# Kernel tuning notes

Hardware: AMD Instinct MI355X
Metric: run time of the kernel (lower is better)

## Reference

```python
import jax, jax.numpy as jnp
from jax import lax
import numpy as np

B, D, T, H = 256, 128, 1024, 64


def setup_inputs() -> dict:
    key = jax.random.key(0)
    ks = jax.random.split(key, 8)
    s = 1.0 / np.sqrt(H)
    latent_chunk = jax.random.normal(ks[0], (B, D, T), dtype=jnp.float32)
    hidden = jnp.zeros((1, B, H), dtype=jnp.float32)
    # PyTorch nn.GRU params: weight_ih [3H, D], weight_hh [3H, H], biases [3H]
    W_ih = jax.random.uniform(ks[1], (3 * H, D), minval=-s, maxval=s, dtype=jnp.float32)
    W_hh = jax.random.uniform(ks[2], (3 * H, H), minval=-s, maxval=s, dtype=jnp.float32)
    b_ih = jax.random.uniform(ks[3], (3 * H,), minval=-s, maxval=s, dtype=jnp.float32)
    b_hh = jax.random.uniform(ks[4], (3 * H,), minval=-s, maxval=s, dtype=jnp.float32)
    head_w = jax.random.uniform(ks[5], (1, H), minval=-s, maxval=s, dtype=jnp.float32)
    head_b = jax.random.uniform(ks[6], (1,), minval=-s, maxval=s, dtype=jnp.float32)
    return {"latent_chunk": latent_chunk, "hidden": hidden, "W_ih": W_ih,
            "W_hh": W_hh, "b_ih": b_ih, "b_hh": b_hh,
            "head_w": head_w, "head_b": head_b}


def _gru_forward(latent_chunk, hidden, W_ih, W_hh, b_ih, b_hh, head_w, head_b):
    # [B, D, T] -> [B, T, D]
    x = jnp.transpose(latent_chunk, (0, 2, 1))
    # Precompute input-gate projections once as a big GEMM: [B, T, 3H]
    xg = jnp.einsum('btd,gd->btg', x, W_ih) + b_ih
    xg_t = jnp.transpose(xg, (1, 0, 2))  # [T, B, 3H] for scan
    h0 = hidden[0]  # single layer: [B, H]

    def step(h, xg_step):
        hg = h @ W_hh.T + b_hh  # [B, 3H]
        xr, xz, xn = jnp.split(xg_step, 3, axis=-1)
        hr, hz, hn = jnp.split(hg, 3, axis=-1)
        r = jax.nn.sigmoid(xr + hr)
        z = jax.nn.sigmoid(xz + hz)
        n = jnp.tanh(xn + r * hn)
        h_new = (1.0 - z) * n + z * h
        return h_new, None

    hT, _ = lax.scan(step, h0, xg_t)
    # last output of single-layer GRU == final hidden state
    log_scale = hT @ head_w.T + head_b  # [B, 1]
    return log_scale, hT[None]  # hidden: [1, B, H]


def reference(latent_chunk, hidden, W_ih, W_hh, b_ih, b_hh, head_w, head_b):
    return _gru_forward(latent_chunk, hidden, W_ih, W_hh, b_ih, b_hh, head_w, head_b)
```

## Files before the change

kernel.cpp:

```cpp
#include <hip/hip_runtime.h>

#define B_ 256
#define D_ 128
#define T_ 1024
#define H_ 64
#define G_ 192
#define TILE_T 64
#define NTILES (T_ / TILE_T)
#define XGS 65
#define KC 32
#define WS 194

typedef float f32x4 __attribute__((ext_vector_type(4)));
typedef unsigned long long u64;

__global__ __launch_bounds__(448, 2) void gru_fused(
    const float* __restrict__ lat, const float* __restrict__ hidden_init,
    const float* __restrict__ W_ih, const float* __restrict__ W_hh,
    const float* __restrict__ b_ih, const float* __restrict__ b_hh,
    const float* __restrict__ head_w, const float* __restrict__ head_b,
    float* __restrict__ out)
{
    __shared__ float xg_s[2][G_ * XGS];
    __shared__ float lat_s[D_ * TILE_T];
    __shared__ float w_s[KC * WS];
    __shared__ float h_priv[3][H_];
    __shared__ u64  slot[3][2][H_];
    __shared__ unsigned prod_done[2], cons_done[2], pbar;

    const int b    = blockIdx.x;
    const int tid  = threadIdx.x;
    const int lane = tid & 63;
    const int wid  = tid >> 6;

    if (tid < 2) { prod_done[tid] = 0u; cons_done[tid] = 0u; }
    if (tid == 2) pbar = 0u;
    if (tid < 192) { slot[tid >> 6][0][tid & 63] = 0ull;
                     slot[tid >> 6][1][tid & 63] = 0ull; }
    __syncthreads();

    if (wid < 3) {
        __builtin_amdgcn_s_setprio(1);
        const int j   = lane;
        const int row = wid * H_ + j;
        f32x4 w4[16];
        {
            const f32x4* W = (const f32x4*)(W_hh + (size_t)row * H_);
#pragma unroll
            for (int q = 0; q < 16; ++q) w4[q] = W[q];
        }
        asm volatile("" : "+v"(w4[0]), "+v"(w4[1]), "+v"(w4[2]), "+v"(w4[3]),
                          "+v"(w4[4]), "+v"(w4[5]), "+v"(w4[6]), "+v"(w4[7]),
                          "+v"(w4[8]), "+v"(w4[9]), "+v"(w4[10]), "+v"(w4[11]),
                          "+v"(w4[12]), "+v"(w4[13]), "+v"(w4[14]), "+v"(w4[15]));
        const float bias = b_hh[row];
        const float hw   = (wid == 0) ? head_w[j] : 0.f;
        const int o1 = (wid == 0) ? 1 : 0;
        const int o2 = (wid == 2) ? 1 : 2;
        float h = hidden_init[b * H_ + j];
        unsigned sg = 0;

        for (int k = 0; k < NTILES; ++k) {
            const int s = k & 1;
            const unsigned tgt = 4u * (unsigned)((k >> 1) + 1);
            while (__hip_atomic_load(&prod_done[s], __ATOMIC_ACQUIRE,
                                     __HIP_MEMORY_SCOPE_WORKGROUP) < tgt)
                __builtin_amdgcn_s_sleep(1);
            const float* xr_p = &xg_s[s][(size_t)j * XGS];
            const float* xz_p = &xg_s[s][(size_t)(H_ + j) * XGS];
            const float* xn_p = &xg_s[s][(size_t)(2 * H_ + j) * XGS];

#pragma unroll 2
            for (int t = 0; t < TILE_T; ++t, ++sg) {
                const int par = (int)(sg & 1u);
                h_priv[wid][j] = h;
                float xr = xr_p[t], xz = xz_p[t], xn = xn_p[t];
                const f32x4* h4 = (const f32x4*)h_priv[wid];
                float a0 = 0.f, a1 = 0.f, a2 = 0.f, a3 = 0.f;
#pragma unroll
                for (int q = 0; q < 16; ++q) {
                    f32x4 hv = h4[q];
                    a0 = fmaf(w4[q].x, hv.x, a0); a1 = fmaf(w4[q].y, hv.y, a1);
                    a2 = fmaf(w4[q].z, hv.z, a2); a3 = fmaf(w4[q].w, hv.w, a3);
                }
                float a = ((a0 + a1) + (a2 + a3)) + bias;
                const unsigned want = sg + 1;

                u64 pk = ((u64)want << 32) | (u64)__builtin_bit_cast(unsigned, a);
                __hip_atomic_store(&slot[wid][par][j], pk, __ATOMIC_RELAXED,
                                   __HIP_MEMORY_SCOPE_WORKGROUP);
                u64 v1, v2;
                do {
                    v1 = __hip_atomic_load(&slot[o1][par][j], __ATOMIC_RELAXED,
                                           __HIP_MEMORY_SCOPE_WORKGROUP);
                    v2 = __hip_atomic_load(&slot[o2][par][j], __ATOMIC_RELAXED,
                                           __HIP_MEMORY_SCOPE_WORKGROUP);
                } while ((unsigned)(v1 >> 32) != want || (unsigned)(v2 >> 32) != want);
                float b1 = __builtin_bit_cast(float, (unsigned)v1);
                float b2 = __builtin_bit_cast(float, (unsigned)v2);

                float ar, az, an;
                if (wid == 0)      { ar = a;  az = b1; an = b2; }
                else if (wid == 1) { ar = b1; az = a;  an = b2; }
                else               { ar = b1; az = b2; an = a;  }

                float r   = __builtin_amdgcn_rcpf(1.f + __expf(-(xr + ar)));
                float z   = __builtin_amdgcn_rcpf(1.f + __expf(-(xz + az)));
                float pre = xn + r * an;
                float n   = fmaf(-2.f, __builtin_amdgcn_rcpf(__expf(2.f * pre) + 1.f), 1.f);
                h = fmaf(z, h - n, n);
            }
            if (lane == 0)
                __hip_atomic_fetch_add(&cons_done[s], 1u, __ATOMIC_RELEASE,
                                       __HIP_MEMORY_SCOPE_WORKGROUP);
        }

        if (wid == 0) {
            out[B_ + b * H_ + j] = h;
            float v = h * hw;
#pragma unroll
            for (int off = 32; off > 0; off >>= 1) v += __shfl_down(v, off);
            if (lane == 0) out[b] = v + head_b[0];
        }
    } else {
        const int p  = tid - 192;
        const int tx = p & 7;
        const int gy = p >> 3;
        const float* latb = lat + (size_t)b * (D_ * T_);
        unsigned phase = 0;

        auto psync = [&]() {
            if ((p & 63) == 0)
                __hip_atomic_fetch_add(&pbar, 1u, __ATOMIC_RELEASE,
                                       __HIP_MEMORY_SCOPE_WORKGROUP);
            ++phase;
            while (__hip_atomic_load(&pbar, __ATOMIC_ACQUIRE,
                                     __HIP_MEMORY_SCOPE_WORKGROUP) < 4u * phase) {}
        };

        float bias[6];
#pragma unroll
        for (int i = 0; i < 6; ++i) bias[i] = b_ih[gy * 6 + i];

        for (int k = 0; k < NTILES; ++k) {
            const int s = k & 1, m = k >> 1;
            if (m >= 1) {
                while (__hip_atomic_load(&cons_done[s], __ATOMIC_ACQUIRE,
                                         __HIP_MEMORY_SCOPE_WORKGROUP) < 3u * (unsigned)m)
                    __builtin_amdgcn_s_sleep(1);
            }
            psync();

#pragma unroll
            for (int i = 0; i < 32; ++i) {
                int f = p + 256 * i;
                int d = f >> 6, t = f & 63;
                lat_s[f] = latb[(size_t)d * T_ + k * TILE_T + t];
            }

            float acc[8][6];
#pragma unroll
            for (int jj = 0; jj < 8; ++jj)
#pragma unroll
                for (int i = 0; i < 6; ++i) acc[jj][i] = 0.f;

            for (int kc = 0; kc < D_; kc += KC) {
                psync();
#pragma unroll
                for (int i = 0; i < (G_ * KC) / 256; ++i) {
                    int f = p + 256 * i;
                    int g = f >> 5, kk = f & 31;
                    w_s[kk * WS + g] = W_ih[(size_t)g * D_ + kc + kk];
                }
                psync();
#pragma unroll 4
                for (int kk = 0; kk < KC; ++kk) {
                    f32x4 l0 = *(const f32x4*)&lat_s[(kc + kk) * 64 + tx * 8];
                    f32x4 l1 = *(const f32x4*)&lat_s[(kc + kk) * 64 + tx * 8 + 4];
                    float2 w0 = *(const float2*)&w_s[kk * WS + gy * 6];
                    float2 w1 = *(const float2*)&w_s[kk * WS + gy * 6 + 2];
                    float2 w2 = *(const float2*)&w_s[kk * WS + gy * 6 + 4];
                    float lv[8] = {l0.x, l0.y, l0.z, l0.w, l1.x, l1.y, l1.z, l1.w};
                    float wv[6] = {w0.x, w0.y, w1.x, w1.y, w2.x, w2.y};
#pragma unroll
                    for (int jj = 0; jj < 8; ++jj)
#pragma unroll
                        for (int i = 0; i < 6; ++i)
                            acc[jj][i] = fmaf(lv[jj], wv[i], acc[jj][i]);
                }
            }

            float* xs = xg_s[s];
#pragma unroll
            for (int i = 0; i < 6; ++i)
#pragma unroll
                for (int jj = 0; jj < 8; ++jj)
                    xs[(size_t)(gy * 6 + i) * XGS + tx * 8 + jj] = acc[jj][i] + bias[i];

            if ((p & 63) == 0)
                __hip_atomic_fetch_add(&prod_done[s], 1u, __ATOMIC_RELEASE,
                                       __HIP_MEMORY_SCOPE_WORKGROUP);
        }
    }
}

extern "C" void kernel_launch(void* const* d_in, const int* in_sizes, int n_in,
                              void* d_out, int out_size, void* d_ws, size_t ws_size,
                              hipStream_t stream)
{
    const float* lat   = (const float*)d_in[0];
    const float* hid0  = (const float*)d_in[1];
    const float* W_ih  = (const float*)d_in[2];
    const float* W_hh  = (const float*)d_in[3];
    const float* b_ih  = (const float*)d_in[4];
    const float* b_hh  = (const float*)d_in[5];
    const float* headw = (const float*)d_in[6];
    const float* headb = (const float*)d_in[7];
    float* out = (float*)d_out;

    gru_fused<<<dim3(B_), dim3(448), 0, stream>>>(
        lat, hid0, W_ih, W_hh, b_ih, b_hh, headw, headb, out);
}
```

Before: 454.3 us.

## Push gate partials into per-consumer slots and vectorize FMAs with packed f32x2

The recurrent warps now write their gate partial sums directly into each peer's paired slot, so every consumer reads both values from adjacent locations in its own slot pair. The old scheme had each warp store to its own slot and poll two separate peers. The producer GEMM switches to f32x2 accumulators so the compiler can emit packed FMA, and it halves the W_ih k-chunk size. Recurrent priority rises to 2 and the matvec uses vector f32x4 accumulation. Together these aim to shorten the serial per-step handshake and speed the input projection. The risks are more frequent producer syncs from the smaller chunk, and relying on volatile accesses instead of atomics for ordering.

```diff
diff --git a/kernel.cpp b/kernel.cpp
--- a/kernel.cpp
+++ b/kernel.cpp
@@ -8,10 +8,11 @@
 #define TILE_T 64
 #define NTILES (T_ / TILE_T)
 #define XGS 65
-#define KC 32
+#define KC 16
 #define WS 194
 
 typedef float f32x4 __attribute__((ext_vector_type(4)));
+typedef float f32x2 __attribute__((ext_vector_type(2)));
 typedef unsigned long long u64;
 
 __global__ __launch_bounds__(448, 2) void gru_fused(
@@ -25,7 +26,7 @@
     __shared__ float lat_s[D_ * TILE_T];
     __shared__ float w_s[KC * WS];
     __shared__ float h_priv[3][H_];
-    __shared__ u64  slot[3][2][H_];
+    __shared__ u64  pairs[3][2][H_][2];
     __shared__ unsigned prod_done[2], cons_done[2], pbar;
 
     const int b    = blockIdx.x;
@@ -35,12 +36,11 @@
 
     if (tid < 2) { prod_done[tid] = 0u; cons_done[tid] = 0u; }
     if (tid == 2) pbar = 0u;
-    if (tid < 192) { slot[tid >> 6][0][tid & 63] = 0ull;
-                     slot[tid >> 6][1][tid & 63] = 0ull; }
+    for (int i = tid; i < 3 * 2 * H_ * 2; i += 448) ((u64*)pairs)[i] = 0ull;
     __syncthreads();
 
     if (wid < 3) {
-        __builtin_amdgcn_s_setprio(1);
+        __builtin_amdgcn_s_setprio(2);
         const int j   = lane;
         const int row = wid * H_ + j;
         f32x4 w4[16];
@@ -57,6 +57,12 @@
         const float hw   = (wid == 0) ? head_w[j] : 0.f;
         const int o1 = (wid == 0) ? 1 : 0;
         const int o2 = (wid == 2) ? 1 : 2;
+        const int i1 = (wid < 3 - o1 - wid) ? 0 : 1;
+        const int i2 = (wid < 3 - o2 - wid) ? 0 : 1;
+        volatile u64* wr1 = &pairs[o1][0][j][i1];
+        volatile u64* wr2 = &pairs[o2][0][j][i2];
+        volatile u64* rd  = &pairs[wid][0][j][0];
+        const int pstride = 2 * H_;
         float h = hidden_init[b * H_ + j];
         unsigned sg = 0;
 
@@ -76,25 +82,20 @@
                 h_priv[wid][j] = h;
                 float xr = xr_p[t], xz = xz_p[t], xn = xn_p[t];
                 const f32x4* h4 = (const f32x4*)h_priv[wid];
-                float a0 = 0.f, a1 = 0.f, a2 = 0.f, a3 = 0.f;
-#pragma unroll
-                for (int q = 0; q < 16; ++q) {
-                    f32x4 hv = h4[q];
-                    a0 = fmaf(w4[q].x, hv.x, a0); a1 = fmaf(w4[q].y, hv.y, a1);
-                    a2 = fmaf(w4[q].z, hv.z, a2); a3 = fmaf(w4[q].w, hv.w, a3);
-                }
-                float a = ((a0 + a1) + (a2 + a3)) + bias;
+                f32x4 a4 = {0.f, 0.f, 0.f, 0.f};
+#pragma unroll
+                for (int q = 0; q < 16; ++q)
+                    a4 += w4[q] * h4[q];
+                float a = ((a4.x + a4.y) + (a4.z + a4.w)) + bias;
                 const unsigned want = sg + 1;
 
                 u64 pk = ((u64)want << 32) | (u64)__builtin_bit_cast(unsigned, a);
-                __hip_atomic_store(&slot[wid][par][j], pk, __ATOMIC_RELAXED,
-                                   __HIP_MEMORY_SCOPE_WORKGROUP);
+                wr1[par * pstride] = pk;
+                wr2[par * pstride] = pk;
                 u64 v1, v2;
                 do {
-                    v1 = __hip_atomic_load(&slot[o1][par][j], __ATOMIC_RELAXED,
-                                           __HIP_MEMORY_SCOPE_WORKGROUP);
-                    v2 = __hip_atomic_load(&slot[o2][par][j], __ATOMIC_RELAXED,
-                                           __HIP_MEMORY_SCOPE_WORKGROUP);
+                    v1 = rd[par * pstride + 0];
+                    v2 = rd[par * pstride + 1];
                 } while ((unsigned)(v1 >> 32) != want || (unsigned)(v2 >> 32) != want);
                 float b1 = __builtin_bit_cast(float, (unsigned)v1);
                 float b2 = __builtin_bit_cast(float, (unsigned)v2);
@@ -158,18 +159,18 @@
                 lat_s[f] = latb[(size_t)d * T_ + k * TILE_T + t];
             }
 
-            float acc[8][6];
-#pragma unroll
-            for (int jj = 0; jj < 8; ++jj)
-#pragma unroll
-                for (int i = 0; i < 6; ++i) acc[jj][i] = 0.f;
+            f32x2 acc2[4][6];
+#pragma unroll
+            for (int jj = 0; jj < 4; ++jj)
+#pragma unroll
+                for (int i = 0; i < 6; ++i) acc2[jj][i] = f32x2{0.f, 0.f};
 
             for (int kc = 0; kc < D_; kc += KC) {
                 psync();
 #pragma unroll
                 for (int i = 0; i < (G_ * KC) / 256; ++i) {
                     int f = p + 256 * i;
-                    int g = f >> 5, kk = f & 31;
+                    int g = f >> 4, kk = f & 15;
                     w_s[kk * WS + g] = W_ih[(size_t)g * D_ + kc + kk];
                 }
                 psync();
@@ -177,16 +178,17 @@
                 for (int kk = 0; kk < KC; ++kk) {
                     f32x4 l0 = *(const f32x4*)&lat_s[(kc + kk) * 64 + tx * 8];
                     f32x4 l1 = *(const f32x4*)&lat_s[(kc + kk) * 64 + tx * 8 + 4];
+                    f32x2 lv2[4] = {f32x2{l0.x, l0.y}, f32x2{l0.z, l0.w},
+                                    f32x2{l1.x, l1.y}, f32x2{l1.z, l1.w}};
                     float2 w0 = *(const float2*)&w_s[kk * WS + gy * 6];
                     float2 w1 = *(const float2*)&w_s[kk * WS + gy * 6 + 2];
                     float2 w2 = *(const float2*)&w_s[kk * WS + gy * 6 + 4];
-                    float lv[8] = {l0.x, l0.y, l0.z, l0.w, l1.x, l1.y, l1.z, l1.w};
                     float wv[6] = {w0.x, w0.y, w1.x, w1.y, w2.x, w2.y};
 #pragma unroll
-                    for (int jj = 0; jj < 8; ++jj)
+                    for (int jj = 0; jj < 4; ++jj)
 #pragma unroll
                         for (int i = 0; i < 6; ++i)
-                            acc[jj][i] = fmaf(lv[jj], wv[i], acc[jj][i]);
+                            acc2[jj][i] += lv2[jj] * f32x2{wv[i], wv[i]};
                 }
             }
 
@@ -194,8 +196,10 @@
 #pragma unroll
             for (int i = 0; i < 6; ++i)
 #pragma unroll
-                for (int jj = 0; jj < 8; ++jj)
-                    xs[(size_t)(gy * 6 + i) * XGS + tx * 8 + jj] = acc[jj][i] + bias[i];
+                for (int jj = 0; jj < 4; ++jj) {
+                    xs[(size_t)(gy * 6 + i) * XGS + tx * 8 + 2 * jj + 0] = acc2[jj][i].x + bias[i];
+                    xs[(size_t)(gy * 6 + i) * XGS + tx * 8 + 2 * jj + 1] = acc2[jj][i].y + bias[i];
+                }
 
             if ((p & 63) == 0)
                 __hip_atomic_fetch_add(&prod_done[s], 1u, __ATOMIC_RELEASE,
```

Measured after the change: 538.4 us. 1.19x slower.
